# Optimization experiments

Hardware: AMD Instinct MI355X
Metric: run time of the kernel (lower is better)

## Reference

```python
import jax, jax.numpy as jnp
import numpy as np

EPS = 1e-5  # BatchNorm eps (torch default)

def setup_inputs() -> dict:
    key = jax.random.key(0)
    ks = jax.random.split(key, 12)
    B, C, H, W = 4, 256, 64, 64
    IC = 128  # inter_channels = C // 2
    s = 1.0 / np.sqrt(C)
    si = 1.0 / np.sqrt(IC)
    return {
        "x": jax.random.normal(ks[0], (B, C, H, W), jnp.float32),
        "y": jax.random.normal(ks[1], (B, C, H, W), jnp.float32),
        "g_w": jax.random.normal(ks[2], (IC, C), jnp.float32) * s,
        "g_b": jax.random.normal(ks[3], (IC,), jnp.float32) * 0.01,
        "dx_w": jax.random.normal(ks[4], (IC, C), jnp.float32) * s,
        "dx_b": jax.random.normal(ks[5], (IC,), jnp.float32) * 0.01,
        "dy_w": jax.random.normal(ks[6], (IC, C), jnp.float32) * s,
        "dy_b": jax.random.normal(ks[7], (IC,), jnp.float32) * 0.01,
        "w_w": jax.random.normal(ks[8], (C, IC), jnp.float32) * si,
        "w_b": jax.random.normal(ks[9], (C,), jnp.float32) * 0.01,
        "bn_gamma": jax.random.normal(ks[10], (C,), jnp.float32),
        "bn_beta": jax.random.normal(ks[11], (C,), jnp.float32) * 0.01,
    }

def _conv1x1(t, w, b):
    # t: [B,C,H,W], w: [O,C], b: [O] -> [B,O,H,W]
    return jnp.einsum('bchw,oc->bohw', t, w) + b[None, :, None, None]

def reference(x, y, g_w, g_b, dx_w, dx_b, dy_w, dy_b, w_w, w_b, bn_gamma, bn_beta):
    B, C, H, W = x.shape
    IC = g_w.shape[0]
    N = H * W
    g_y = _conv1x1(y, g_w, g_b).reshape(B, IC, N).transpose(0, 2, 1)      # [B,N,IC]
    theta_x = _conv1x1(x, dx_w, dx_b).reshape(B, IC, N).transpose(0, 2, 1)  # [B,N,IC]
    phi_y = _conv1x1(y, dy_w, dy_b).reshape(B, IC, N)                      # [B,IC,N]
    f = jnp.einsum('bnc,bcm->bnm', theta_x, phi_y)                         # [B,N,N]
    f_div_C = jax.nn.softmax(f, axis=-1)
    y2 = jnp.einsum('bnm,bmc->bnc', f_div_C, g_y)                          # [B,N,IC]
    y2 = y2.transpose(0, 2, 1).reshape(B, IC, H, W)
    wy = _conv1x1(y2, w_w, w_b)                                            # [B,C,H,W]
    # BatchNorm2d in training mode: batch stats over (B,H,W) per channel
    mean = jnp.mean(wy, axis=(0, 2, 3), keepdims=True)
    var = jnp.var(wy, axis=(0, 2, 3), keepdims=True)
    wy_bn = (wy - mean) / jnp.sqrt(var + EPS)
    wy_bn = wy_bn * bn_gamma[None, :, None, None] + bn_beta[None, :, None, None]
    return wy_bn + x
```

## Files before the change

kernel.cpp:

```cpp
#include <hip/hip_runtime.h>
#include <hip/hip_bf16.h>
#include <math.h>

typedef unsigned short ushort_t;
typedef __attribute__((ext_vector_type(8))) short     short8;
typedef __attribute__((ext_vector_type(8))) _Float16  half8;
typedef __attribute__((ext_vector_type(8))) unsigned short ushort8;
typedef __attribute__((ext_vector_type(4))) float     float4v;
typedef __attribute__((ext_vector_type(16))) float    floatx16;

__device__ __forceinline__ float b2f(ushort_t u) {
    return __uint_as_float(((unsigned)u) << 16);
}
__device__ __forceinline__ ushort_t f2b(float f) {
    unsigned i = __float_as_uint(f);
    return (ushort_t)((i + 0x7FFFu + ((i >> 16) & 1u)) >> 16);
}
__device__ __forceinline__ void split2(float v, ushort_t& h, ushort_t& l) {
    h = f2b(v);
    l = f2b(v - b2f(h));
}
__device__ __forceinline__ void glds16(const ushort_t* g, ushort_t* l) {
    __builtin_amdgcn_global_load_lds((const __attribute__((address_space(1))) void*)g,
                                     (__attribute__((address_space(3))) void*)l, 16, 0, 0);
}
__device__ __forceinline__ unsigned int pack2bf(float lo, float hi) {
    unsigned int r;
    asm("v_cvt_pk_bf16_f32 %0, %1, %2" : "=v"(r) : "v"(lo), "v"(hi));
    return r;
}
__device__ __forceinline__ void pl32swap(unsigned int& a, unsigned int& b) {
    asm("v_permlane32_swap_b32 %0, %1" : "+v"(a), "+v"(b));
}

#define WTFH_OFF   0
#define WTFL_OFF   196608
#define WWBH_OFF   393216
#define WWBL_OFF   458752
#define BIAS_OFF   524288
#define STATS_OFF  526336
#define PROJF_OFF  1048576
#define GT_OFF     9437184
#define OPART_OFF  13631488
#define WY_OFF     1048576

__global__ void prep_k(const float* __restrict__ dx_w, const float* __restrict__ dy_w,
                       const float* __restrict__ g_w,  const float* __restrict__ dx_b,
                       const float* __restrict__ dy_b, const float* __restrict__ g_b,
                       const float* __restrict__ w_w,
                       ushort_t* __restrict__ wtfh, ushort_t* __restrict__ wtfl,
                       ushort_t* __restrict__ wwbh, ushort_t* __restrict__ wwbl,
                       float* __restrict__ bias) {
    int idx = blockIdx.x * 256 + threadIdx.x;
    int j = idx & 7, lane = (idx >> 3) & 63, kk = (idx >> 9) & 7, ot = idx >> 12;
    int o = ot * 16 + (lane & 15);
    int c = kk * 32 + ((lane >> 4) * 8) + j;
    float v;
    if (o < 128)      v = dx_w[o * 256 + c];
    else if (o < 256) v = dy_w[(o - 128) * 256 + c];
    else              v = g_w[(o - 256) * 256 + c];
    ushort_t h, l;
    split2(v, h, l);
    wtfh[idx] = h; wtfl[idx] = l;
    if (idx < 32768) {
        split2(w_w[idx], h, l);
        wwbh[idx] = h; wwbl[idx] = l;
    }
    if (idx < 384) {
        bias[idx] = (idx < 128) ? dx_b[idx]
                  : (idx < 256) ? dy_b[idx - 128]
                                : g_b[idx - 256];
    }
}

#define XTS 258
__global__ __launch_bounds__(256) void proj_k(const float* __restrict__ x,
                                              const float* __restrict__ y,
                                              const ushort_t* __restrict__ wtfh,
                                              const ushort_t* __restrict__ wtfl,
                                              const float* __restrict__ bias,
                                              ushort_t* __restrict__ projf,
                                              ushort_t* __restrict__ gT) {
    __shared__ ushort_t xT[2][32 * XTS];
    int b = blockIdx.y, n0 = blockIdx.x * 32;
    int tid = threadIdx.x;
    int w = tid >> 6, lane = tid & 63;
    int mrow = lane & 15, quad = lane >> 4, koff = quad * 8;
    int half = w & 1, sect = w >> 1;
    int arow = half * 16 + mrow;

    for (int s = 0; s < 2; s++) {
        if (s) __syncthreads();
        const float* src = s ? y : x;
        #pragma unroll
        for (int i = 0; i < 4; i++) {
            int ch = tid + i * 256;
            int c = ch >> 2, off = (ch & 3) * 8;
            const float* p = src + (size_t)(b * 256 + c) * 4096 + n0 + off;
            float4v v0 = *(const float4v*)p;
            float4v v1 = *(const float4v*)(p + 4);
            #pragma unroll
            for (int jj = 0; jj < 4; jj++) {
                ushort_t h, l;
                split2(v0[jj], h, l);
                xT[0][(off + jj) * XTS + c] = h;
                xT[1][(off + jj) * XTS + c] = l;
                split2(v1[jj], h, l);
                xT[0][(off + 4 + jj) * XTS + c] = h;
                xT[1][(off + 4 + jj) * XTS + c] = l;
            }
        }
        __syncthreads();

        short8 fh[8], fl[8];
        #pragma unroll
        for (int kk = 0; kk < 8; kk++) {
            fh[kk] = *(const short8*)&xT[0][arow * XTS + kk * 32 + koff];
            fl[kk] = *(const short8*)&xT[1][arow * XTS + kk * 32 + koff];
        }

        int ot0 = s ? (8 + sect * 8) : (sect * 4);
        int ot1 = s ? (ot0 + 8) : (ot0 + 4);
        for (int ot = ot0; ot < ot1; ot++) {
            float4v acc = {0.f, 0.f, 0.f, 0.f};
            #pragma unroll
            for (int kk = 0; kk < 8; kk++) {
                short8 bh = *(const short8*)(wtfh + (size_t)((ot * 8 + kk) * 64 + lane) * 8);
                short8 bl = *(const short8*)(wtfl + (size_t)((ot * 8 + kk) * 64 + lane) * 8);
                acc = __builtin_amdgcn_mfma_f32_16x16x32_bf16(fh[kk], bh, acc, 0, 0, 0);
                acc = __builtin_amdgcn_mfma_f32_16x16x32_bf16(fh[kk], bl, acc, 0, 0, 0);
                acc = __builtin_amdgcn_mfma_f32_16x16x32_bf16(fl[kk], bh, acc, 0, 0, 0);
            }
            int o = ot * 16 + mrow;
            float bo = bias[o];
            #pragma unroll
            for (int r = 0; r < 4; r++) {
                int n = n0 + half * 16 + quad * 4 + r;
                float v = acc[r] + bo;
                if (ot < 16) {
                    _Float16 hf = (_Float16)v;
                    projf[(size_t)(b * 4096 + n) * 256 + o] = *(ushort_t*)&hf;
                } else {
                    gT[(size_t)(b * 128 + (o - 256)) * 4096 + n] = f2b(v);
                }
            }
        }
    }
}

template<int KVB>
__global__ __launch_bounds__(256, (KVB == 32 ? 4 : 2))
void flash_k(const ushort_t* __restrict__ projf,
             const ushort_t* __restrict__ gT,
             float* __restrict__ opart,
             float* __restrict__ oml,
             int kqlog) {
    constexpr int NT2 = KVB / 32;
    constexpr int NCH = KVB / 4;
    constexpr int NPT = NCH / 4;
    __shared__ __align__(16) ushort_t KsF[2][KVB * 128];
    __shared__ __align__(16) ushort_t VsF[2][KVB * 128];

    int L = blockIdx.x;
    int xcd = L & 7, t = L >> 3;
    int c, j;
    if (kqlog >= 2)      { c = (t >> 5) * 8 + xcd; j = t & 31; }
    else if (kqlog == 1) { c = xcd;                j = t; }
    else                 { c = xcd & 3;            j = t + ((xcd >> 2) << 4); }
    int b  = c >> kqlog;
    int kq = c & ((1 << kqlog) - 1);
    int q0 = j * 128;
    int iters = (4096 >> kqlog) / KVB;
    int kt0 = kq * iters;
    int tid = threadIdx.x, w = tid >> 6, lane = tid & 63;
    int ln = lane & 31, hh = lane >> 5;

    const ushort_t* kSrc[NPT];
    const ushort_t* vSrc[NPT];
    {
        int kb0 = kt0 * KVB;
        #pragma unroll
        for (int i = 0; i < NPT; i++) {
            int cc = w + i * 4;
            int t2 = cc >> 3, kk = cc & 7;
            kSrc[i] = projf + (size_t)(b * 4096 + kb0 + t2 * 32 + ln) * 256 + 128 + kk * 16 + hh * 8;
            int it = cc / (2 * NT2), g = cc % (2 * NT2);
            vSrc[i] = gT + (size_t)(b * 128 + it * 32 + ln) * 4096 + kb0 + g * 16 + hh * 8;
        }
    }

    half8 qf[8];
    {
        const ushort_t* qp = projf + (size_t)(b * 4096 + q0 + w * 32 + ln) * 256 + hh * 8;
        #pragma unroll
        for (int kk = 0; kk < 8; kk++)
            qf[kk] = *(const half8*)(qp + kk * 16);
    }

    floatx16 oacc[4];
    #pragma unroll
    for (int it = 0; it < 4; it++)
        #pragma unroll
        for (int jj = 0; jj < 16; jj++) oacc[it][jj] = 0.f;
    float lacc[NT2];
    #pragma unroll
    for (int t2 = 0; t2 < NT2; t2++) lacc[t2] = 0.f;

    #pragma unroll
    for (int i = 0; i < NPT; i++) {
        int cc = w + i * 4;
        glds16(kSrc[i], &KsF[0][cc * 512]);
        glds16(vSrc[i], &VsF[0][cc * 512]);
        kSrc[i] += (size_t)KVB * 256;
        vSrc[i] += KVB;
    }

    for (int kt = kt0; kt < kt0 + iters; kt++) {
        int cur = (kt - kt0) & 1;
        __syncthreads();
        if (kt + 1 < kt0 + iters) {
            #pragma unroll
            for (int i = 0; i < NPT; i++) {
                int cc = w + i * 4;
                glds16(kSrc[i], &KsF[1 - cur][cc * 512]);
                glds16(vSrc[i], &VsF[1 - cur][cc * 512]);
                kSrc[i] += (size_t)KVB * 256;
                vSrc[i] += KVB;
            }
        }

        floatx16 sacc[NT2];
        #pragma unroll
        for (int t2 = 0; t2 < NT2; t2++)
            #pragma unroll
            for (int jj = 0; jj < 16; jj++) sacc[t2][jj] = 0.f;
        __builtin_amdgcn_s_setprio(1);
        #pragma unroll
        for (int kk = 0; kk < 8; kk++) {
            #pragma unroll
            for (int t2 = 0; t2 < NT2; t2++) {
                half8 ah = *(const half8*)&KsF[cur][((t2 * 8 + kk) * 64 + lane) * 8];
                sacc[t2] = __builtin_amdgcn_mfma_f32_32x32x16_f16(ah, qf[kk], sacc[t2], 0, 0, 0);
            }
        }
        __builtin_amdgcn_s_setprio(0);

        short8 fr[2 * NT2];
        #pragma unroll
        for (int t2 = 0; t2 < NT2; t2++) {
            float ps[16];
            #pragma unroll
            for (int r = 0; r < 16; r++)
                ps[r] = __builtin_exp2f(fmaf(sacc[t2][r], 1.44269504f, -92.332481f));
            lacc[t2] += ((((ps[0] + ps[1]) + (ps[2] + ps[3]))
                        + ((ps[4] + ps[5]) + (ps[6] + ps[7])))
                       + (((ps[8] + ps[9]) + (ps[10] + ps[11]))
                        + ((ps[12] + ps[13]) + (ps[14] + ps[15]))));
            unsigned int pw[8];
            #pragma unroll
            for (int c2 = 0; c2 < 8; c2++) pw[c2] = pack2bf(ps[2 * c2], ps[2 * c2 + 1]);
            pl32swap(pw[0], pw[2]);
            pl32swap(pw[1], pw[3]);
            pl32swap(pw[4], pw[6]);
            pl32swap(pw[5], pw[7]);
            union { unsigned int u[4]; short8 s8; } fA, fB;
            fA.u[0] = pw[0]; fA.u[1] = pw[1]; fA.u[2] = pw[2]; fA.u[3] = pw[3];
            fB.u[0] = pw[4]; fB.u[1] = pw[5]; fB.u[2] = pw[6]; fB.u[3] = pw[7];
            fr[t2 * 2]     = fA.s8;
            fr[t2 * 2 + 1] = fB.s8;
        }

        __builtin_amdgcn_s_setprio(1);
        #pragma unroll
        for (int it = 0; it < 4; it++) {
            #pragma unroll
            for (int kg = 0; kg < 2 * NT2; kg++) {
                short8 vv = *(const short8*)&VsF[cur][((it * 2 * NT2 + kg) * 64 + lane) * 8];
                oacc[it] = __builtin_amdgcn_mfma_f32_32x32x16_bf16(fr[kg], vv, oacc[it], 0, 0, 0);
            }
        }
        __builtin_amdgcn_s_setprio(0);
    }

    {
        int rowBase = b * 4096 + q0 + w * 32 + hh * 4;
        #pragma unroll
        for (int it = 0; it < 4; it++)
            #pragma unroll
            for (int r = 0; r < 16; r++) {
                int qrow = rowBase + (r & 3) + 8 * (r >> 2);
                opart[((size_t)kq * 16384 + qrow) * 128 + it * 32 + ln] = oacc[it][r];
            }
    }
    float lsum = lacc[0];
    #pragma unroll
    for (int t2 = 1; t2 < NT2; t2++) lsum += lacc[t2];
    lsum += __shfl_xor(lsum, 32, 64);
    if (lane < 32)
        oml[kq * 16384 + b * 4096 + q0 + w * 32 + lane] = lsum;
}

__global__ __launch_bounds__(256) void wy_k(const float* __restrict__ opart,
                                            const float* __restrict__ oml,
                                            const ushort_t* __restrict__ wwbh,
                                            const ushort_t* __restrict__ wwbl,
                                            const float* __restrict__ w_b,
                                            ushort_t* __restrict__ wy, int KQ) {
    int b = blockIdx.y, n0 = blockIdx.x * 32;
    int tid = threadIdx.x, w = tid >> 6, lane = tid & 63;
    int mrow = lane & 15, quad = lane >> 4, koff = quad * 8;
    int half = w & 1, sect = w >> 1;
    int Rn = b * 4096 + n0 + half * 16 + mrow;

    float L = 0.f;
    for (int kq = 0; kq < KQ; kq++) L += oml[kq * 16384 + Rn];
    float invL = 1.f / L;

    short8 bfh[4], bfl[4];
    #pragma unroll
    for (int kk = 0; kk < 4; kk++) {
        float a[8];
        #pragma unroll
        for (int j = 0; j < 8; j++) a[j] = 0.f;
        for (int kq = 0; kq < KQ; kq++) {
            const float* p = opart + ((size_t)kq * 16384 + Rn) * 128 + kk * 32 + koff;
            float4v v0 = *(const float4v*)p;
            float4v v1 = *(const float4v*)(p + 4);
            #pragma unroll
            for (int j = 0; j < 4; j++) { a[j] += v0[j]; a[4 + j] += v1[j]; }
        }
        #pragma unroll
        for (int j = 0; j < 8; j++) {
            ushort_t h, l;
            split2(a[j] * invL, h, l);
            bfh[kk][j] = (short)h; bfl[kk][j] = (short)l;
        }
    }

    int coln = n0 + half * 16 + mrow;
    for (int cot = sect * 8; cot < sect * 8 + 8; cot++) {
        float4v acc = {0.f, 0.f, 0.f, 0.f};
        #pragma unroll
        for (int kk = 0; kk < 4; kk++) {
            size_t woff = (size_t)(cot * 16 + mrow) * 128 + kk * 32 + koff;
            short8 ah = *(const short8*)(wwbh + woff);
            short8 al = *(const short8*)(wwbl + woff);
            acc = __builtin_amdgcn_mfma_f32_16x16x32_bf16(ah, bfh[kk], acc, 0, 0, 0);
            acc = __builtin_amdgcn_mfma_f32_16x16x32_bf16(ah, bfl[kk], acc, 0, 0, 0);
            acc = __builtin_amdgcn_mfma_f32_16x16x32_bf16(al, bfh[kk], acc, 0, 0, 0);
        }
        #pragma unroll
        for (int r = 0; r < 4; r++) {
            int co = cot * 16 + quad * 4 + r;
            wy[(size_t)(b * 256 + co) * 4096 + coln] = f2b(acc[r] + w_b[co]);
        }
    }
}

__global__ __launch_bounds__(256) void stats_k(const ushort_t* __restrict__ wy,
                                               float* __restrict__ stats) {
    __shared__ float red[8];
    int co = blockIdx.x, tid = threadIdx.x, w = tid >> 6, lane = tid & 63;
    float s = 0.f, s2 = 0.f;
    #pragma unroll
    for (int i = 0; i < 8; i++) {
        int ch = tid + i * 256;
        int b = ch >> 9, n = (ch & 511) * 8;
        ushort8 v = *(const ushort8*)(wy + (size_t)(b * 256 + co) * 4096 + n);
        #pragma unroll
        for (int j = 0; j < 8; j++) { float f = b2f(v[j]); s += f; s2 += f * f; }
    }
    #pragma unroll
    for (int d = 1; d < 64; d <<= 1) { s += __shfl_xor(s, d, 64); s2 += __shfl_xor(s2, d, 64); }
    if (lane == 0) { red[w] = s; red[4 + w] = s2; }
    __syncthreads();
    if (tid == 0) {
        stats[co]       = red[0] + red[1] + red[2] + red[3];
        stats[256 + co] = red[4] + red[5] + red[6] + red[7];
    }
}

__global__ __launch_bounds__(256) void bn_k(const ushort_t* __restrict__ wy,
                                            const float* __restrict__ x,
                                            const float* __restrict__ gamma,
                                            const float* __restrict__ beta,
                                            const float* __restrict__ stats,
                                            float* __restrict__ out) {
    int idx = (blockIdx.x * 256 + threadIdx.x) * 8;
    int c = (idx >> 12) & 255;
    const float inv_cnt = 1.f / 16384.f;
    float mean = stats[c] * inv_cnt;
    float var  = stats[256 + c] * inv_cnt - mean * mean;
    float inv  = rsqrtf(var + 1e-5f);
    float scale = gamma[c] * inv;
    float shift = beta[c] - mean * scale;
    ushort8 wv = *(const ushort8*)(wy + idx);
    float4v x0 = *(const float4v*)(x + idx);
    float4v x1 = *(const float4v*)(x + idx + 4);
    float4v o0, o1;
    #pragma unroll
    for (int j = 0; j < 4; j++) {
        o0[j] = b2f(wv[j]) * scale + shift + x0[j];
        o1[j] = b2f(wv[4 + j]) * scale + shift + x1[j];
    }
    *(float4v*)(out + idx) = o0;
    *(float4v*)(out + idx + 4) = o1;
}

extern "C" void kernel_launch(void* const* d_in, const int* in_sizes, int n_in,
                              void* d_out, int out_size, void* d_ws, size_t ws_size,
                              hipStream_t stream) {
    const float* x    = (const float*)d_in[0];
    const float* y    = (const float*)d_in[1];
    const float* g_w  = (const float*)d_in[2];
    const float* g_b  = (const float*)d_in[3];
    const float* dx_w = (const float*)d_in[4];
    const float* dx_b = (const float*)d_in[5];
    const float* dy_w = (const float*)d_in[6];
    const float* dy_b = (const float*)d_in[7];
    const float* w_w  = (const float*)d_in[8];
    const float* w_b  = (const float*)d_in[9];
    const float* bn_g = (const float*)d_in[10];
    const float* bn_b = (const float*)d_in[11];

    char* ws = (char*)d_ws;
    ushort_t* wtfh  = (ushort_t*)(ws + WTFH_OFF);
    ushort_t* wtfl  = (ushort_t*)(ws + WTFL_OFF);
    ushort_t* wwbh  = (ushort_t*)(ws + WWBH_OFF);
    ushort_t* wwbl  = (ushort_t*)(ws + WWBL_OFF);
    float*    bias  = (float*)(ws + BIAS_OFF);
    float*    stats = (float*)(ws + STATS_OFF);
    ushort_t* projf = (ushort_t*)(ws + PROJF_OFF);
    ushort_t* gT    = (ushort_t*)(ws + GT_OFF);
    float*    opart = (float*)(ws + OPART_OFF);
    ushort_t* wy    = (ushort_t*)(ws + WY_OFF);
    float*    out   = (float*)d_out;

    int kqlog;
    if      (ws_size >= 13631488u + 8u * (8388608u + 65536u)) kqlog = 3;
    else if (ws_size >= 13631488u + 4u * (8388608u + 65536u)) kqlog = 2;
    else if (ws_size >= 13631488u + 2u * (8388608u + 65536u)) kqlog = 1;
    else                                                      kqlog = 0;
    int KQ = 1 << kqlog;
    float* oml = (float*)(ws + OPART_OFF + (size_t)KQ * 8388608u);

    prep_k<<<384, 256, 0, stream>>>(dx_w, dy_w, g_w, dx_b, dy_b, g_b, w_w,
                                    wtfh, wtfl, wwbh, wwbl, bias);
    proj_k<<<dim3(128, 4), 256, 0, stream>>>(x, y, wtfh, wtfl, bias, projf, gT);
    if (kqlog == 3)
        flash_k<32><<<dim3(1024), 256, 0, stream>>>(projf, gT, opart, oml, 3);
    else
        flash_k<64><<<dim3(128 << kqlog), 256, 0, stream>>>(projf, gT, opart, oml, kqlog);
    wy_k<<<dim3(128, 4), 256, 0, stream>>>(opart, oml, wwbh, wwbl, w_b, wy, KQ);
    stats_k<<<256, 256, 0, stream>>>(wy, stats);
    bn_k<<<2048, 256, 0, stream>>>(wy, x, bn_g, bn_b, stats, out);
}
```

Baseline: 242.1 us.

## Fuse BatchNorm statistics into wy kernel via atomics and cap key split

Removes the separate stats_k pass by accumulating per-channel sum and sum-of-squares inside wy_k. Each tile is reduced with wave shuffles and then added to global stats with atomicAdd, and the stats buffer is zeroed in prep_k. It also drops the KQ=8 flash_k<32> variant, so at most 4 key partitions are used, which shrinks the opart traffic that wy_k has to read. The cost is atomic contention on 512 floats, nondeterministic summation order, and less parallelism in the flash stage.

```diff
diff --git a/kernel.cpp b/kernel.cpp
--- a/kernel.cpp
+++ b/kernel.cpp
@@ -50,7 +50,7 @@
                        const float* __restrict__ w_w,
                        ushort_t* __restrict__ wtfh, ushort_t* __restrict__ wtfl,
                        ushort_t* __restrict__ wwbh, ushort_t* __restrict__ wwbl,
-                       float* __restrict__ bias) {
+                       float* __restrict__ bias, float* __restrict__ stats) {
     int idx = blockIdx.x * 256 + threadIdx.x;
     int j = idx & 7, lane = (idx >> 3) & 63, kk = (idx >> 9) & 7, ot = idx >> 12;
     int o = ot * 16 + (lane & 15);
@@ -71,6 +71,7 @@
                   : (idx < 256) ? dy_b[idx - 128]
                                 : g_b[idx - 256];
     }
+    if (idx < 512) stats[idx] = 0.f;
 }
 
 #define XTS 258
@@ -305,7 +306,8 @@
                                             const ushort_t* __restrict__ wwbh,
                                             const ushort_t* __restrict__ wwbl,
                                             const float* __restrict__ w_b,
-                                            ushort_t* __restrict__ wy, int KQ) {
+                                            ushort_t* __restrict__ wy,
+                                            float* __restrict__ stats, int KQ) {
     int b = blockIdx.y, n0 = blockIdx.x * 32;
     int tid = threadIdx.x, w = tid >> 6, lane = tid & 63;
     int mrow = lane & 15, quad = lane >> 4, koff = quad * 8;
@@ -349,34 +351,31 @@
             acc = __builtin_amdgcn_mfma_f32_16x16x32_bf16(ah, bfl[kk], acc, 0, 0, 0);
             acc = __builtin_amdgcn_mfma_f32_16x16x32_bf16(al, bfh[kk], acc, 0, 0, 0);
         }
+        float s1v[4], s2v[4];
         #pragma unroll
         for (int r = 0; r < 4; r++) {
             int co = cot * 16 + quad * 4 + r;
-            wy[(size_t)(b * 256 + co) * 4096 + coln] = f2b(acc[r] + w_b[co]);
-        }
-    }
-}
-
-__global__ __launch_bounds__(256) void stats_k(const ushort_t* __restrict__ wy,
-                                               float* __restrict__ stats) {
-    __shared__ float red[8];
-    int co = blockIdx.x, tid = threadIdx.x, w = tid >> 6, lane = tid & 63;
-    float s = 0.f, s2 = 0.f;
-    #pragma unroll
-    for (int i = 0; i < 8; i++) {
-        int ch = tid + i * 256;
-        int b = ch >> 9, n = (ch & 511) * 8;
-        ushort8 v = *(const ushort8*)(wy + (size_t)(b * 256 + co) * 4096 + n);
-        #pragma unroll
-        for (int j = 0; j < 8; j++) { float f = b2f(v[j]); s += f; s2 += f * f; }
-    }
-    #pragma unroll
-    for (int d = 1; d < 64; d <<= 1) { s += __shfl_xor(s, d, 64); s2 += __shfl_xor(s2, d, 64); }
-    if (lane == 0) { red[w] = s; red[4 + w] = s2; }
-    __syncthreads();
-    if (tid == 0) {
-        stats[co]       = red[0] + red[1] + red[2] + red[3];
-        stats[256 + co] = red[4] + red[5] + red[6] + red[7];
+            ushort_t bv = f2b(acc[r] + w_b[co]);
+            wy[(size_t)(b * 256 + co) * 4096 + coln] = bv;
+            float vb = b2f(bv);
+            s1v[r] = vb; s2v[r] = vb * vb;
+        }
+        #pragma unroll
+        for (int d = 1; d < 16; d <<= 1) {
+            #pragma unroll
+            for (int r = 0; r < 4; r++) {
+                s1v[r] += __shfl_xor(s1v[r], d, 64);
+                s2v[r] += __shfl_xor(s2v[r], d, 64);
+            }
+        }
+        if (mrow == 0) {
+            #pragma unroll
+            for (int r = 0; r < 4; r++) {
+                int co = cot * 16 + quad * 4 + r;
+                atomicAdd(&stats[co],       s1v[r]);
+                atomicAdd(&stats[256 + co], s2v[r]);
+            }
+        }
     }
 }
 
@@ -437,21 +436,16 @@
     float*    out   = (float*)d_out;
 
     int kqlog;
-    if      (ws_size >= 13631488u + 8u * (8388608u + 65536u)) kqlog = 3;
-    else if (ws_size >= 13631488u + 4u * (8388608u + 65536u)) kqlog = 2;
+    if      (ws_size >= 13631488u + 4u * (8388608u + 65536u)) kqlog = 2;
     else if (ws_size >= 13631488u + 2u * (8388608u + 65536u)) kqlog = 1;
     else                                                      kqlog = 0;
     int KQ = 1 << kqlog;
     float* oml = (float*)(ws + OPART_OFF + (size_t)KQ * 8388608u);
 
     prep_k<<<384, 256, 0, stream>>>(dx_w, dy_w, g_w, dx_b, dy_b, g_b, w_w,
-                                    wtfh, wtfl, wwbh, wwbl, bias);
+                                    wtfh, wtfl, wwbh, wwbl, bias, stats);
     proj_k<<<dim3(128, 4), 256, 0, stream>>>(x, y, wtfh, wtfl, bias, projf, gT);
-    if (kqlog == 3)
-        flash_k<32><<<dim3(1024), 256, 0, stream>>>(projf, gT, opart, oml, 3);
-    else
-        flash_k<64><<<dim3(128 << kqlog), 256, 0, stream>>>(projf, gT, opart, oml, kqlog);
-    wy_k<<<dim3(128, 4), 256, 0, stream>>>(opart, oml, wwbh, wwbl, w_b, wy, KQ);
-    stats_k<<<256, 256, 0, stream>>>(wy, stats);
+    flash_k<64><<<dim3(128 << kqlog), 256, 0, stream>>>(projf, gT, opart, oml, kqlog);
+    wy_k<<<dim3(128, 4), 256, 0, stream>>>(opart, oml, wwbh, wwbl, w_b, wy, stats, KQ);
     bn_k<<<2048, 256, 0, stream>>>(wy, x, bn_g, bn_b, stats, out);
 }
```

New measurement: 371.8 us. +53.6%, slower.

## Split split-K merge into separate kernel and cap flash split at four

Applied to the files above, without the earlier changes.

Moves the reduction of the split-K partial attention outputs, normalisation and bf16 hi/lo split out of the wy GEMM kernel into a dedicated, fully parallel elementwise merge kernel templated on KQ. The wy GEMM then reads the precomputed bf16 operands directly. The KQ=8 path with flash_k<32> is dropped, so the largest split is now four, using flash_k<64>. The aim is to spread the memory-bound merge over many more threads instead of the 512-block GEMM. The cost is an extra launch and an extra intermediate round-trip through memory.

```diff
diff --git a/kernel.cpp b/kernel.cpp
--- a/kernel.cpp
+++ b/kernel.cpp
@@ -6,6 +6,7 @@
 typedef __attribute__((ext_vector_type(8))) short     short8;
 typedef __attribute__((ext_vector_type(8))) _Float16  half8;
 typedef __attribute__((ext_vector_type(8))) unsigned short ushort8;
+typedef __attribute__((ext_vector_type(4))) unsigned short ushort4v;
 typedef __attribute__((ext_vector_type(4))) float     float4v;
 typedef __attribute__((ext_vector_type(16))) float    floatx16;
 
@@ -42,7 +43,9 @@
 #define PROJF_OFF  1048576
 #define GT_OFF     9437184
 #define OPART_OFF  13631488
-#define WY_OFF     1048576
+#define Y2H_OFF    1048576
+#define Y2L_OFF    5242880
+#define WY_OFF     13631488
 
 __global__ void prep_k(const float* __restrict__ dx_w, const float* __restrict__ dy_w,
                        const float* __restrict__ g_w,  const float* __restrict__ dx_b,
@@ -300,41 +303,51 @@
         oml[kq * 16384 + b * 4096 + q0 + w * 32 + lane] = lsum;
 }
 
-__global__ __launch_bounds__(256) void wy_k(const float* __restrict__ opart,
-                                            const float* __restrict__ oml,
-                                            const ushort_t* __restrict__ wwbh,
-                                            const ushort_t* __restrict__ wwbl,
-                                            const float* __restrict__ w_b,
-                                            ushort_t* __restrict__ wy, int KQ) {
+template<int KQ>
+__global__ __launch_bounds__(256) void merge_k(const float* __restrict__ opart,
+                                               const float* __restrict__ oml,
+                                               ushort_t* __restrict__ y2h,
+                                               ushort_t* __restrict__ y2l) {
+    int f = blockIdx.x * 256 + threadIdx.x;
+    int R = f >> 5;
+    float L = 0.f;
+    #pragma unroll
+    for (int kq = 0; kq < KQ; kq++) L += oml[kq * 16384 + R];
+    float invL = 1.f / L;
+    float a[4] = {0.f, 0.f, 0.f, 0.f};
+    #pragma unroll
+    for (int kq = 0; kq < KQ; kq++) {
+        float4v v = *(const float4v*)(opart + (size_t)kq * 2097152 + (size_t)f * 4);
+        a[0] += v[0]; a[1] += v[1]; a[2] += v[2]; a[3] += v[3];
+    }
+    ushort4v hv, lv;
+    #pragma unroll
+    for (int j = 0; j < 4; j++) {
+        ushort_t h, l;
+        split2(a[j] * invL, h, l);
+        hv[j] = h; lv[j] = l;
+    }
+    *(ushort4v*)(y2h + (size_t)f * 4) = hv;
+    *(ushort4v*)(y2l + (size_t)f * 4) = lv;
+}
+
+__global__ __launch_bounds__(256) void wy_gemm(const ushort_t* __restrict__ y2h,
+                                               const ushort_t* __restrict__ y2l,
+                                               const ushort_t* __restrict__ wwbh,
+                                               const ushort_t* __restrict__ wwbl,
+                                               const float* __restrict__ w_b,
+                                               ushort_t* __restrict__ wy) {
     int b = blockIdx.y, n0 = blockIdx.x * 32;
     int tid = threadIdx.x, w = tid >> 6, lane = tid & 63;
     int mrow = lane & 15, quad = lane >> 4, koff = quad * 8;
     int half = w & 1, sect = w >> 1;
     int Rn = b * 4096 + n0 + half * 16 + mrow;
 
-    float L = 0.f;
-    for (int kq = 0; kq < KQ; kq++) L += oml[kq * 16384 + Rn];
-    float invL = 1.f / L;
-
     short8 bfh[4], bfl[4];
     #pragma unroll
     for (int kk = 0; kk < 4; kk++) {
-        float a[8];
-        #pragma unroll
-        for (int j = 0; j < 8; j++) a[j] = 0.f;
-        for (int kq = 0; kq < KQ; kq++) {
-            const float* p = opart + ((size_t)kq * 16384 + Rn) * 128 + kk * 32 + koff;
-            float4v v0 = *(const float4v*)p;
-            float4v v1 = *(const float4v*)(p + 4);
-            #pragma unroll
-            for (int j = 0; j < 4; j++) { a[j] += v0[j]; a[4 + j] += v1[j]; }
-        }
-        #pragma unroll
-        for (int j = 0; j < 8; j++) {
-            ushort_t h, l;
-            split2(a[j] * invL, h, l);
-            bfh[kk][j] = (short)h; bfl[kk][j] = (short)l;
-        }
+        bfh[kk] = *(const short8*)(y2h + (size_t)Rn * 128 + kk * 32 + koff);
+        bfl[kk] = *(const short8*)(y2l + (size_t)Rn * 128 + kk * 32 + koff);
     }
 
     int coln = n0 + half * 16 + mrow;
@@ -433,12 +446,13 @@
     ushort_t* projf = (ushort_t*)(ws + PROJF_OFF);
     ushort_t* gT    = (ushort_t*)(ws + GT_OFF);
     float*    opart = (float*)(ws + OPART_OFF);
+    ushort_t* y2h   = (ushort_t*)(ws + Y2H_OFF);
+    ushort_t* y2l   = (ushort_t*)(ws + Y2L_OFF);
     ushort_t* wy    = (ushort_t*)(ws + WY_OFF);
     float*    out   = (float*)d_out;
 
     int kqlog;
-    if      (ws_size >= 13631488u + 8u * (8388608u + 65536u)) kqlog = 3;
-    else if (ws_size >= 13631488u + 4u * (8388608u + 65536u)) kqlog = 2;
+    if      (ws_size >= 13631488u + 4u * (8388608u + 65536u)) kqlog = 2;
     else if (ws_size >= 13631488u + 2u * (8388608u + 65536u)) kqlog = 1;
     else                                                      kqlog = 0;
     int KQ = 1 << kqlog;
@@ -447,11 +461,14 @@
     prep_k<<<384, 256, 0, stream>>>(dx_w, dy_w, g_w, dx_b, dy_b, g_b, w_w,
                                     wtfh, wtfl, wwbh, wwbl, bias);
     proj_k<<<dim3(128, 4), 256, 0, stream>>>(x, y, wtfh, wtfl, bias, projf, gT);
-    if (kqlog == 3)
-        flash_k<32><<<dim3(1024), 256, 0, stream>>>(projf, gT, opart, oml, 3);
+    flash_k<64><<<dim3(128 << kqlog), 256, 0, stream>>>(projf, gT, opart, oml, kqlog);
+    if (KQ == 4)
+        merge_k<4><<<2048, 256, 0, stream>>>(opart, oml, y2h, y2l);
+    else if (KQ == 2)
+        merge_k<2><<<2048, 256, 0, stream>>>(opart, oml, y2h, y2l);
     else
-        flash_k<64><<<dim3(128 << kqlog), 256, 0, stream>>>(projf, gT, opart, oml, kqlog);
-    wy_k<<<dim3(128, 4), 256, 0, stream>>>(opart, oml, wwbh, wwbl, w_b, wy, KQ);
+        merge_k<1><<<2048, 256, 0, stream>>>(opart, oml, y2h, y2l);
+    wy_gemm<<<dim3(128, 4), 256, 0, stream>>>(y2h, y2l, wwbh, wwbl, w_b, wy);
     stats_k<<<256, 256, 0, stream>>>(wy, stats);
     bn_k<<<2048, 256, 0, stream>>>(wy, x, bn_g, bn_b, stats, out);
 }
```

New measurement: 221.2 us. 8.7% less time.
